# Kernel optimization log

Hardware: AMD Instinct MI355X
Metric: run time of the kernel (lower is better)

Reference implementation:

```python
import jax, jax.numpy as jnp
import numpy as np


def setup_inputs() -> dict:
    key = jax.random.key(0)
    kz, kh, k0 = jax.random.split(key, 3)
    B, C, D, H, W = 2, 96, 32, 32, 32
    z = jax.random.uniform(kz, (B, C, D, H, W), dtype=jnp.float32)  # gate in [0,1]
    h_tilde = jax.random.normal(kh, (B, C, D, H, W), dtype=jnp.float32)  # candidate state
    h0 = jax.random.uniform(k0, (1,), dtype=jnp.float32)  # scalar initial state
    return {"z": z, "h_tilde": h_tilde, "h0": h0}


def reference(z, h_tilde, h0):
    """GruDirection3d with d1=d2=d3=1 (forward_3, no flips).

    The three wavefront slice-updates in the torch code jointly implement
        out[d, y, x] = z[d, y, x] * h_tilde[d, y, x]
                       + (1 - z[d, y, x]) * out[d-1, y-1, x-1]
    with out == h0 whenever any index goes below 0 (the padded border).
    We realize it as t_num = min(D, H, W) full-volume shifted updates: after
    iteration k, all voxels with min(d, y, x) <= k-1 hold their final value,
    so after t_num iterations the result matches the torch wavefront DP exactly.
    """
    B, C, D, H, W = z.shape
    t_num = min(D, H, W)  # static shapes -> python int, jit-safe
    # padded state: index 0 along each spatial axis is the h0 border (never written)
    h_pad = jnp.full((B, C, D + 1, H + 1, W + 1), h0[0], dtype=z.dtype)

    one = jnp.asarray(1, dtype=z.dtype)

    def step(h_pad, _):
        prev = h_pad[:, :, :-1, :-1, :-1]  # out[d-1, y-1, x-1] (with border = h0)
        new = z * h_tilde + (one - z) * prev
        return h_pad.at[:, :, 1:, 1:, 1:].set(new), None

    h_pad, _ = jax.lax.scan(step, h_pad, None, length=t_num)
    return h_pad[:, :, 1:, 1:, 1:]
```

## Files before the change

kernel.cpp:

```cpp
#include <hip/hip_runtime.h>


#define DD 32
#define PF 8

__global__ __launch_bounds__(256) void gru3d_helix(
    const float* __restrict__ z,
    const float* __restrict__ ht,
    const float* __restrict__ h0p,
    float* __restrict__ out)
{
    const int blk  = blockIdx.x;
    const int slab = blk >> 2;
    const int agrp = blk & 3;
    const int tid  = threadIdx.x;
    const int a    = (agrp << 3) + (tid >> 5);
    const int b    = tid & 31;

    const float h0 = h0p[0];

    const size_t base = (size_t)slab * (DD * 1024);
    const float* __restrict__ zb = z   + base;
    const float* __restrict__ tb = ht  + base;
    float*       __restrict__ ob = out + base;

    auto off = [&](int d) -> int {
        return (d << 10) | (((a + d) & 31) << 5) | ((b + d) & 31);
    };

    float zr[PF], tr[PF];
    #pragma unroll
    for (int p = 0; p < PF; ++p) {
        zr[p] = zb[off(p)];
        tr[p] = tb[off(p)];
    }

    float h = h0;

    #pragma unroll
    for (int d = 0; d < DD; ++d) {
        const int s = d & (PF - 1);

        const bool border = (((a + d) & 31) == 0) | (((b + d) & 31) == 0);
        const float pred  = border ? h0 : h;

        h = zr[s] * (tr[s] - pred) + pred;
        ob[off(d)] = h;

        if (d + PF < DD) {
            zr[s] = zb[off(d + PF)];
            tr[s] = tb[off(d + PF)];
        }
    }
}

extern "C" void kernel_launch(void* const* d_in, const int* in_sizes, int n_in,
                              void* d_out, int out_size, void* d_ws, size_t ws_size,
                              hipStream_t stream) {
    const float* z  = (const float*)d_in[0];
    const float* ht = (const float*)d_in[1];
    const float* h0 = (const float*)d_in[2];
    float* out      = (float*)d_out;

    const int BC = 2 * 96;
    gru3d_helix<<<dim3(BC * 4), dim3(256), 0, stream>>>(z, ht, h0, out);
}
```

Baseline: 92.59 us.

## Process two x-voxels per thread with float2 accesses and lane shuffles

```diff
diff --git a/kernel.cpp b/kernel.cpp
--- a/kernel.cpp
+++ b/kernel.cpp
@@ -4,7 +4,7 @@
 #define DD 32
 #define PF 8
 
-__global__ __launch_bounds__(256) void gru3d_helix(
+__global__ __launch_bounds__(128) void gru3d_helix_f2(
     const float* __restrict__ z,
     const float* __restrict__ ht,
     const float* __restrict__ h0p,
@@ -12,10 +12,10 @@
 {
     const int blk  = blockIdx.x;
     const int slab = blk >> 2;
-    const int agrp = blk & 3;
+    const int band = blk & 3;
     const int tid  = threadIdx.x;
-    const int a    = (agrp << 3) + (tid >> 5);
-    const int b    = tid & 31;
+    const int a    = (band << 3) + (tid >> 4);
+    const int bg   = tid & 15;
 
     const float h0 = h0p[0];
 
@@ -25,31 +25,37 @@
     float*       __restrict__ ob = out + base;
 
     auto off = [&](int d) -> int {
-        return (d << 10) | (((a + d) & 31) << 5) | ((b + d) & 31);
+        return (d << 10) | (((a + d) & 31) << 5) | (bg << 1);
     };
 
-    float zr[PF], tr[PF];
+    float2 zr[PF], tr[PF];
     #pragma unroll
     for (int p = 0; p < PF; ++p) {
-        zr[p] = zb[off(p)];
-        tr[p] = tb[off(p)];
+        zr[p] = *reinterpret_cast<const float2*>(zb + off(p));
+        tr[p] = *reinterpret_cast<const float2*>(tb + off(p));
     }
 
-    float h = h0;
+    float hx = h0, hy = h0;
 
     #pragma unroll
     for (int d = 0; d < DD; ++d) {
         const int s = d & (PF - 1);
 
-        const bool border = (((a + d) & 31) == 0) | (((b + d) & 31) == 0);
-        const float pred  = border ? h0 : h;
+        const float n = __shfl_up(hy, 1);
 
-        h = zr[s] * (tr[s] - pred) + pred;
-        ob[off(d)] = h;
+        float px = (bg == 0) ? h0 : n;
+        float py = hx;
+        const bool yb = (d == 0) | (((a + d) & 31) == 0);
+        if (yb) { px = h0; py = h0; }
+
+        hx = zr[s].x * (tr[s].x - px) + px;
+        hy = zr[s].y * (tr[s].y - py) + py;
+
+        *reinterpret_cast<float2*>(ob + off(d)) = make_float2(hx, hy);
 
         if (d + PF < DD) {
-            zr[s] = zb[off(d + PF)];
-            tr[s] = tb[off(d + PF)];
+            zr[s] = *reinterpret_cast<const float2*>(zb + off(d + PF));
+            tr[s] = *reinterpret_cast<const float2*>(tb + off(d + PF));
         }
     }
 }
@@ -63,5 +69,5 @@
     float* out      = (float*)d_out;
 
     const int BC = 2 * 96;
-    gru3d_helix<<<dim3(BC * 4), dim3(256), 0, stream>>>(z, ht, h0, out);
+    gru3d_helix_f2<<<dim3(BC * 4), dim3(128), 0, stream>>>(z, ht, h0, out);
 }
```

Measured after the change: 94.94 us. 1.03x slower.
